# Performance work log

Measured on AMD Instinct MI355X. Metric: run time of the kernel, lower is better.

Reference implementation:

```python
import jax, jax.numpy as jnp
import numpy as np

EPS = 1e-12
B, C, H, M, E, P = 2, 20000, 64, 8, 200000, 3


def setup_inputs() -> dict:
    key = jax.random.key(0)
    ks = jax.random.split(key, 24)
    inp = {}
    inp["features"] = jax.random.normal(ks[0], (B, C, H), jnp.float32)
    inp["positions"] = jax.random.normal(ks[1], (B, C, P), jnp.float32)
    inp["edge_index"] = jax.random.randint(ks[2], (2, E), 0, C)
    inp["degree"] = jax.random.randint(ks[3], (C,), 1, 33).astype(jnp.float32)
    inp["cell_node_indices"] = jax.random.randint(ks[4], (C, M), 0, C)
    mask = (jax.random.uniform(ks[5], (C, M)) > 0.3).astype(jnp.float32)
    inp["cell_node_mask"] = mask.at[:, 0].set(1.0)  # first node always valid (pad semantics)

    def lin(k, fan_in, fan_out):
        return (jax.random.normal(k, (fan_in, fan_out), jnp.float32) / np.sqrt(fan_in)).astype(jnp.float32)

    # message MLP: Linear(2H+4 -> H), SiLU, Linear(H -> H)
    inp["W1"] = lin(ks[6], 2 * H + 4, H); inp["b1"] = jnp.zeros((H,), jnp.float32)
    inp["W2"] = lin(ks[7], H, H);         inp["b2"] = jnp.zeros((H,), jnp.float32)
    # position MLP: Linear(H -> H), SiLU, Linear(H -> 1)
    inp["P1"] = lin(ks[8], H, H);  inp["pb1"] = jnp.zeros((H,), jnp.float32)
    inp["P2"] = lin(ks[9], H, 1);  inp["pb2"] = jnp.zeros((1,), jnp.float32)
    # update MLP: Linear(2H -> H), SiLU, Linear(H -> H)
    inp["U1"] = lin(ks[10], 2 * H, H); inp["ub1"] = jnp.zeros((H,), jnp.float32)
    inp["U2"] = lin(ks[11], H, H);     inp["ub2"] = jnp.zeros((H,), jnp.float32)
    return inp


def _mlp(x, Wa, ba, Wb, bb):
    return jax.nn.silu(x @ Wa + ba) @ Wb + bb


def _forward(features, positions, edge_index, degree, cell_node_indices, cell_node_mask,
             W1, b1, W2, b2, P1, pb1, P2, pb2, U1, ub1, U2, ub2):
    src, dst = edge_index[0], edge_index[1]
    # gather padded node positions per cell: [B, C, M, P]
    node_pos = positions[:, cell_node_indices]

    h_src = features[:, src]                      # [B,E,H]
    h_dst = features[:, dst]
    rel = positions[:, src] - positions[:, dst]   # [B,E,P]
    dist = jnp.linalg.norm(rel, axis=-1, keepdims=True)  # [B,E,1]

    sp = node_pos[:, src]                         # [B,E,M,P]
    dp = node_pos[:, dst]
    mx = cell_node_mask[src]                      # [E,M]
    my = cell_node_mask[dst]

    # pairwise distances [B,E,M,M] via gram trick (avoids [B,E,M,M,P] intermediate)
    sp2 = jnp.sum(sp * sp, -1)                    # [B,E,M]
    dp2 = jnp.sum(dp * dp, -1)
    cross = jnp.einsum('bemp,benp->bemn', sp, dp)
    d = jnp.sqrt(jnp.maximum(sp2[..., :, None] + dp2[..., None, :] - 2.0 * cross, 0.0) + EPS)

    # masked pairwise-distance sum
    w = mx[:, :, None] * my[:, None, :]           # [E,M,M]
    pairwise = jnp.sum(d * w[None], axis=(-1, -2))  # [B,E]

    # centroid distance
    denx = jnp.maximum(mx.sum(-1, keepdims=True), EPS)  # [E,1]
    deny = jnp.maximum(my.sum(-1, keepdims=True), EPS)
    cx = jnp.sum(sp * mx[None, :, :, None], axis=2) / denx[None]  # [B,E,P]
    cy = jnp.sum(dp * my[None, :, :, None], axis=2) / deny[None]
    centroid = jnp.linalg.norm(cx - cy, axis=-1)  # [B,E]

    # Hausdorff distance (masked min/max)
    inf = jnp.float32(jnp.inf)
    d_xy = jnp.where(my[None, :, None, :] <= 0, inf, d)
    min_xy = jnp.where(mx[None] <= 0, 0.0, d_xy.min(-1))  # [B,E,M]
    h_xy = min_xy.max(-1)                                  # [B,E]
    d_yx = jnp.where(mx[None, :, None, :] <= 0, inf, jnp.swapaxes(d, -1, -2))
    min_yx = jnp.where(my[None] <= 0, 0.0, d_yx.min(-1))
    h_yx = min_yx.max(-1)
    haus = jnp.maximum(h_xy, h_yx)

    invariants = jnp.concatenate([dist, pairwise[..., None], centroid[..., None], haus[..., None]], -1)  # [B,E,4]
    msg_in = jnp.concatenate([h_src, h_dst, invariants], -1)  # [B,E,2H+4]
    messages = _mlp(msg_in, W1, b1, W2, b2)                   # [B,E,H]

    # scatter-aggregate into destination cells, degree-normalize
    agg = jnp.zeros_like(features).at[:, dst].add(messages)
    agg = agg / jnp.maximum(degree, 1.0)[None, :, None]

    # position update
    wts = jnp.tanh(_mlp(messages, P1, pb1, P2, pb2))          # [B,E,1]
    pos_upd = jnp.zeros_like(positions).at[:, dst].add(wts * rel)

    new_features = features + _mlp(jnp.concatenate([features, agg], -1), U1, ub1, U2, ub2)
    new_positions = positions + pos_upd
    return new_features, new_positions


def reference(features, positions, edge_index, degree, cell_node_indices, cell_node_mask,
              W1, b1, W2, b2, P1, pb1, P2, pb2, U1, ub1, U2, ub2):
    return _forward(features, positions, edge_index, degree, cell_node_indices, cell_node_mask,
                    W1, b1, W2, b2, P1, pb1, P2, pb2, U1, ub1, U2, ub2)
```

## Files before the change

kernel.cpp:

```cpp
#include <hip/hip_runtime.h>
#include <hip/hip_bf16.h>

#define B_ 2
#define C_ 20000
#define H_ 64
#define M_ 8
#define E_ 200000
#define P_ 3
#define EPS_ 1e-12f
#define ET_ (E_ / 64)

typedef __attribute__((ext_vector_type(8))) short short8;
typedef __attribute__((ext_vector_type(4))) float float4v;

__device__ __forceinline__ float silu_(float x) {
    return x / (1.f + __expf(-x));
}
__device__ __forceinline__ float tanh_fast_(float x) {
    float ex = __expf(2.f * x);
    return 1.f - 2.f / (ex + 1.f);
}
__device__ __forceinline__ unsigned short f2b(float f) {
    unsigned u = __float_as_uint(f);
    unsigned r = (u + 0x7FFF + ((u >> 16) & 1)) >> 16;
    return (unsigned short)r;
}
__device__ __forceinline__ float b2f(unsigned short h) {
    return __uint_as_float(((unsigned)h) << 16);
}
__device__ __forceinline__ unsigned pk2u(float a, float b) {
    __hip_bfloat162 h = __float22bfloat162_rn(make_float2(a, b));
    unsigned u; __builtin_memcpy(&u, &h, sizeof(u)); return u;
}
__device__ __forceinline__ float4 up4_(const unsigned short* p) {
    uint2 u = *(const uint2*)p;
    return make_float4(__uint_as_float(u.x << 16),
                       __uint_as_float(u.x & 0xffff0000u),
                       __uint_as_float(u.y << 16),
                       __uint_as_float(u.y & 0xffff0000u));
}

#define W1S_OFF 0
#define W2S_OFF 8192
#define P1S_OFF 12288
#define U1S_OFF 16384
#define U2S_OFF 24576
#define WBUF_ELEMS 28672

#define NB_PREP   120
#define NB_FEATB  2500
#define NB_DESC   157
#define NB_HIST   782
#define NB_COMBO  (NB_PREP + NB_FEATB + NB_DESC + NB_HIST)

#define NB_GEOM   6250
#define NB_AGGZ   2500
#define NB_PCPY   118
#define NB_GEOMK  (NB_GEOM + NB_AGGZ + NB_PCPY)

__global__ __launch_bounds__(256) void combo_kernel(
    const float* __restrict__ W1, const float* __restrict__ W2,
    const float* __restrict__ P1, const float* __restrict__ U1,
    const float* __restrict__ U2, unsigned short* __restrict__ wbuf,
    const float* __restrict__ feat, unsigned short* __restrict__ featb,
    const float* __restrict__ pos, const int* __restrict__ cni,
    const float* __restrict__ mask, unsigned short* __restrict__ descb,
    const int* __restrict__ ei, int* __restrict__ cnt)
{
    const int bid = blockIdx.x;
    if (bid < NB_PREP) {
        int t = bid * 256 + threadIdx.x;
        if (t >= WBUF_ELEMS) return;
        const float* W; int e;
        if (t < W2S_OFF)      { W = W1; e = t; }
        else if (t < U1S_OFF) { W = (t < P1S_OFF) ? W2 : P1; e = (t < P1S_OFF) ? t - W2S_OFF : t - P1S_OFF; }
        else if (t < U2S_OFF) { W = U1; e = t - U1S_OFF; }
        else                  { W = U2; e = t - U2S_OFF; }
        int j = e & 7, lane = (e >> 3) & 63, nt = (e >> 9) & 3, kk = e >> 11;
        int k = kk * 32 + ((lane >> 4) * 8) + j;
        int n = nt * 16 + (lane & 15);
        wbuf[t] = f2b(W[k * 64 + n]);
    } else if (bid < NB_PREP + NB_FEATB) {
        int t = (bid - NB_PREP) * 256 + threadIdx.x;
        float4 v = *(const float4*)&feat[(size_t)t * 4];
        *(uint2*)&featb[(size_t)t * 4] = make_uint2(pk2u(v.x, v.y), pk2u(v.z, v.w));
    } else if (bid < NB_PREP + NB_FEATB + NB_DESC) {
        int tid = (bid - NB_PREP - NB_FEATB) * 256 + threadIdx.x;
        if (tid >= B_ * C_) return;
        int b = tid / C_, c = tid - b * C_;
        const float* pb = pos + (size_t)b * C_ * P_;
        unsigned short* R = descb + (size_t)tid * 40;
        int4 n0 = *(const int4*)&cni[c*8];
        int4 n1 = *(const int4*)&cni[c*8 + 4];
        float4 m0 = *(const float4*)&mask[c*8];
        float4 m1 = *(const float4*)&mask[c*8 + 4];
        int ni[8] = {n0.x, n0.y, n0.z, n0.w, n1.x, n1.y, n1.z, n1.w};
        float mm[8] = {m0.x, m0.y, m0.z, m0.w, m1.x, m1.y, m1.z, m1.w};
        float sx = 0.f, sy = 0.f, sz = 0.f, sm = 0.f;
        #pragma unroll
        for (int m = 0; m < 8; ++m) {
            float x = pb[ni[m]*3+0], y = pb[ni[m]*3+1], z = pb[ni[m]*3+2];
            *(uint2*)&R[m*4] = make_uint2(pk2u(x, y), pk2u(z, mm[m]));
            sx += x * mm[m]; sy += y * mm[m]; sz += z * mm[m]; sm += mm[m];
        }
        float inv = 1.f / fmaxf(sm, EPS_);
        *(uint2*)&R[32] = make_uint2(pk2u(sx*inv, sy*inv), pk2u(sz*inv, sm));
        *(uint2*)&R[36] = make_uint2(pk2u(pb[c*3+0], pb[c*3+1]), pk2u(pb[c*3+2], 0.f));
    } else {
        int e = (bid - NB_PREP - NB_FEATB - NB_DESC) * 256 + threadIdx.x;
        if (e >= E_) return;
        atomicAdd(&cnt[ei[E_ + e]], 1);
    }
}

__global__ __launch_bounds__(256) void alloc_kernel(
    const int* __restrict__ cnt, int* __restrict__ cursor, int* __restrict__ total)
{
    int idx = blockIdx.x * 256 + threadIdx.x;
    int lane = threadIdx.x & 63;
    int v = (idx < C_) ? cnt[idx] : 0;
    int inc = v;
    #pragma unroll
    for (int s = 1; s < 64; s <<= 1) {
        int n = __shfl_up(inc, s);
        if (lane >= s) inc += n;
    }
    int wtot = __shfl(inc, 63);
    int base = 0;
    if (lane == 0) base = atomicAdd(total, wtot);
    base = __shfl(base, 0);
    if (idx < C_) cursor[idx] = base + inc - v;
}

__global__ __launch_bounds__(256) void scatter_kernel(
    const int* __restrict__ ei, int* __restrict__ cursor,
    int2* __restrict__ sedge)
{
    int e = blockIdx.x * 256 + threadIdx.x;
    if (e >= E_) return;
    int s = ei[e], d = ei[E_ + e];
    int slot = atomicAdd(&cursor[d], 1);
    sedge[slot] = make_int2(s, d);
}

__global__ __launch_bounds__(256) void geom_kernel(
    const int2* __restrict__ sedge, const unsigned short* __restrict__ descb,
    float* __restrict__ inv8,
    float* __restrict__ aggf, const float* __restrict__ pos,
    float* __restrict__ out_pos)
{
    const int bid = blockIdx.x;
    if (bid >= NB_GEOM) {
        if (bid < NB_GEOM + NB_AGGZ) {
            int t = (bid - NB_GEOM) * 256 + threadIdx.x;
            ((float4*)aggf)[t] = make_float4(0.f, 0.f, 0.f, 0.f);
        } else {
            int t = (bid - NB_GEOM - NB_AGGZ) * 256 + threadIdx.x;
            if (t < (B_ * C_ * P_) / 4)
                ((float4*)out_pos)[t] = ((const float4*)pos)[t];
        }
        return;
    }
    const int tid  = threadIdx.x;
    const int w    = tid >> 6;
    const int lane = tid & 63;
    const int q    = lane >> 4;
    const int l16  = lane & 15;

    const int ge = bid * 64 + w * 16 + l16;
    const int b  = ge / E_;
    const int i  = ge - b * E_;
    const int2 sd = sedge[i];
    const unsigned short* Sb = descb + ((size_t)b * C_ + sd.x) * 40;
    const unsigned short* Db = descb + ((size_t)b * C_ + sd.y) * 40;

    const float INFV = __builtin_inff();
    float4 S[8];
    float a_i[8], infm_i[8], rowmin[8];
    #pragma unroll
    for (int k = 0; k < 8; ++k) {
        S[k] = up4_(&Sb[k*4]);
        a_i[k] = S[k].x*S[k].x + S[k].y*S[k].y + S[k].z*S[k].z + EPS_;
        infm_i[k] = (S[k].w > 0.f) ? 0.f : INFV;
        rowmin[k] = INFV;
    }
    float pair = 0.f, hyx = 0.f;
    #pragma unroll
    for (int jj = 0; jj < 2; ++jj) {
        float4 Dj = up4_(&Db[(q*2 + jj)*4]);
        float dp2 = Dj.x*Dj.x + Dj.y*Dj.y + Dj.z*Dj.z;
        float infm_j = (Dj.w > 0.f) ? 0.f : INFV;
        float colmin = INFV, psum = 0.f;
        #pragma unroll
        for (int k = 0; k < 8; ++k) {
            float cr = S[k].x*Dj.x + S[k].y*Dj.y + S[k].z*Dj.z;
            float t  = (a_i[k] + dp2) - 2.f*cr;
            float dd = sqrtf(fmaxf(t, EPS_));
            psum = fmaf(dd, S[k].w, psum);
            rowmin[k] = fminf(rowmin[k], dd + infm_j);
            colmin    = fminf(colmin,    dd + infm_i[k]);
        }
        pair = fmaf(Dj.w, psum, pair);
        hyx = fmaxf(hyx, (Dj.w > 0.f) ? colmin : 0.f);
    }
    pair += __shfl_xor(pair, 16);  pair += __shfl_xor(pair, 32);
    hyx = fmaxf(hyx, __shfl_xor(hyx, 16));  hyx = fmaxf(hyx, __shfl_xor(hyx, 32));
    #pragma unroll
    for (int k = 0; k < 8; ++k) {
        rowmin[k] = fminf(rowmin[k], __shfl_xor(rowmin[k], 16));
        rowmin[k] = fminf(rowmin[k], __shfl_xor(rowmin[k], 32));
    }
    float hxy = 0.f;
    #pragma unroll
    for (int k = 0; k < 8; ++k)
        hxy = fmaxf(hxy, (S[k].w > 0.f) ? rowmin[k] : 0.f);

    float4 Sc = up4_(&Sb[32]), Dc = up4_(&Db[32]);
    float cdx = Sc.x - Dc.x, cdy = Sc.y - Dc.y, cdz = Sc.z - Dc.z;
    float4 Sp = up4_(&Sb[36]), Dp = up4_(&Db[36]);
    float relx = Sp.x - Dp.x, rely = Sp.y - Dp.y, relz = Sp.z - Dp.z;
    float dist = sqrtf(relx*relx + rely*rely + relz*relz);
    float cen  = sqrtf(cdx*cdx + cdy*cdy + cdz*cdz);
    float haus = fmaxf(hxy, hyx);

    size_t off = ((size_t)b * E_ + i) * 8;
    if (q == 0)      *(float4*)&inv8[off]     = make_float4(dist, pair, cen, haus);
    else if (q == 1) *(float4*)&inv8[off + 4] = make_float4(relx, rely, relz, 0.f);
}

__global__ __launch_bounds__(256) void edge_kernel(
    const unsigned short* __restrict__ featb,
    const int2* __restrict__ sedge, const float* __restrict__ inv8,
    const unsigned short* __restrict__ wbuf, const float* __restrict__ W1,
    const float* __restrict__ b1, const float* __restrict__ b2,
    const float* __restrict__ pb1, const float* __restrict__ P2,
    const float* __restrict__ pb2,
    float* __restrict__ aggf, float* __restrict__ out_pos)
{
    __shared__ unsigned short lds[4 * 3328];

    const int tid  = threadIdx.x;
    const int w    = tid >> 6;
    const int lane = tid & 63;
    const int q    = lane >> 4;
    const int l16  = lane & 15;
    const int w16  = w * 16;

    const int tile = blockIdx.x;
    const int b    = tile / ET_;
    const int i0   = (tile - b * ET_) * 64;
    const int2 sd  = sedge[i0 + lane];
    const int s_l  = sd.x;
    const int d_l  = sd.y;
    const unsigned short* fb = featb + (size_t)b * C_ * H_;
    const float* ivb = inv8 + ((size_t)b * E_ + i0) * 8;

    unsigned short* Xw = lds + w * 3328;
    unsigned short* Hw = Xw + 2176;
    unsigned short* Mw = Xw;

    float4 ivhi = *(const float4*)&ivb[(w16 + l16) * 8 + 4];
    const float relx = ivhi.x, rely = ivhi.y, relz = ivhi.z;

    const int rr4 = lane >> 4, c4 = lane & 15;
    #pragma unroll
    for (int it = 0; it < 4; ++it) {
        int rloc = it * 4 + rr4;
        int r = w16 + rloc;
        int sr = __shfl(s_l, r);
        int dr = __shfl(d_l, r);
        uint2 vs = *(const uint2*)&fb[(size_t)sr * 64 + c4 * 4];
        uint2 vd = *(const uint2*)&fb[(size_t)dr * 64 + c4 * 4];
        *(uint2*)&Xw[rloc*136 + c4*4]      = vs;
        *(uint2*)&Xw[rloc*136 + 64 + c4*4] = vd;
    }

    float4v acc[4];
    #pragma unroll
    for (int nt = 0; nt < 4; ++nt) {
        float bv = b1[nt*16 + l16];
        acc[nt] = (float4v){bv, bv, bv, bv};
    }
    #pragma unroll
    for (int kk = 0; kk < 4; ++kk) {
        short8 a = *(const short8*)&Xw[l16*136 + kk*32 + q*8];
        #pragma unroll
        for (int nt = 0; nt < 4; ++nt) {
            short8 bf = *(const short8*)&wbuf[W1S_OFF + (((kk*4 + nt)*64) + lane) * 8];
            acc[nt] = __builtin_amdgcn_mfma_f32_16x16x32_bf16(a, bf, acc[nt], 0, 0, 0);
        }
    }
    float4 iv[4];
    #pragma unroll
    for (int i = 0; i < 4; ++i)
        iv[i] = *(const float4*)&ivb[(w16 + q*4 + i) * 8];
    #pragma unroll
    for (int nt = 0; nt < 4; ++nt) {
        float wa = W1[128*64 + nt*16 + l16];
        float wb = W1[129*64 + nt*16 + l16];
        float wc = W1[130*64 + nt*16 + l16];
        float wd = W1[131*64 + nt*16 + l16];
        #pragma unroll
        for (int i = 0; i < 4; ++i)
            acc[nt][i] += iv[i].x*wa + iv[i].y*wb + iv[i].z*wc + iv[i].w*wd;
    }
    #pragma unroll
    for (int nt = 0; nt < 4; ++nt)
        #pragma unroll
        for (int i = 0; i < 4; ++i)
            Hw[(q*4 + i)*72 + nt*16 + l16] = f2b(silu_(acc[nt][i]));

    float4v mac[4];
    #pragma unroll
    for (int nt = 0; nt < 4; ++nt) {
        float bv = b2[nt*16 + l16];
        mac[nt] = (float4v){bv, bv, bv, bv};
    }
    #pragma unroll
    for (int kk = 0; kk < 2; ++kk) {
        short8 a = *(const short8*)&Hw[l16*72 + kk*32 + q*8];
        #pragma unroll
        for (int nt = 0; nt < 4; ++nt) {
            short8 bf = *(const short8*)&wbuf[W2S_OFF + (((kk*4 + nt)*64) + lane) * 8];
            mac[nt] = __builtin_amdgcn_mfma_f32_16x16x32_bf16(a, bf, mac[nt], 0, 0, 0);
        }
    }
    #pragma unroll
    for (int nt = 0; nt < 4; ++nt)
        #pragma unroll
        for (int i = 0; i < 4; ++i)
            Mw[(q*4 + i)*72 + nt*16 + l16] = f2b(mac[nt][i]);

    float4v gac[4];
    #pragma unroll
    for (int nt = 0; nt < 4; ++nt) {
        float bv = pb1[nt*16 + l16];
        gac[nt] = (float4v){bv, bv, bv, bv};
    }
    #pragma unroll
    for (int kk = 0; kk < 2; ++kk) {
        short8 a = *(const short8*)&Mw[l16*72 + kk*32 + q*8];
        #pragma unroll
        for (int nt = 0; nt < 4; ++nt) {
            short8 bf = *(const short8*)&wbuf[P1S_OFF + (((kk*4 + nt)*64) + lane) * 8];
            gac[nt] = __builtin_amdgcn_mfma_f32_16x16x32_bf16(a, bf, gac[nt], 0, 0, 0);
        }
    }
    float p2v[4];
    #pragma unroll
    for (int nt = 0; nt < 4; ++nt) p2v[nt] = P2[nt*16 + l16];
    const float pb2v = pb2[0];

    #pragma unroll
    for (int i = 0; i < 4; ++i) {
        float p = 0.f;
        #pragma unroll
        for (int nt = 0; nt < 4; ++nt) p += silu_(gac[nt][i]) * p2v[nt];
        p += __shfl_xor(p, 8);
        p += __shfl_xor(p, 4);
        p += __shfl_xor(p, 2);
        p += __shfl_xor(p, 1);
        float wt = tanh_fast_(p + pb2v);
        if (l16 == 0) *(float*)&Mw[(q*4 + i)*72 + 64] = wt;
    }

    float* aggB = aggf + (size_t)b * C_ * 64;
    float* opB  = out_pos + (size_t)b * C_ * 3;

    float mrow[16];
    #pragma unroll
    for (int rr = 0; rr < 16; ++rr) mrow[rr] = b2f(Mw[rr*72 + lane]);
    float wtl = *(const float*)&Mw[l16*72 + 64];

    int dprev = __shfl(d_l, w16);
    float colacc = 0.f, pxa = 0.f, pya = 0.f, pza = 0.f;
    #pragma unroll
    for (int rr = 0; rr < 16; ++rr) {
        int dcur = __shfl(d_l, w16 + rr);
        if (dcur != dprev) {
            atomicAdd(&aggB[(size_t)dprev * 64 + lane], colacc);
            if (lane < 3) {
                float v = (lane == 0) ? pxa : (lane == 1) ? pya : pza;
                atomicAdd(&opB[(size_t)dprev * 3 + lane], v);
            }
            colacc = 0.f; pxa = 0.f; pya = 0.f; pza = 0.f;
            dprev = dcur;
        }
        float wt = __shfl(wtl, rr);
        colacc += mrow[rr];
        pxa = fmaf(wt, __shfl(relx, rr), pxa);
        pya = fmaf(wt, __shfl(rely, rr), pya);
        pza = fmaf(wt, __shfl(relz, rr), pza);
    }
    atomicAdd(&aggB[(size_t)dprev * 64 + lane], colacc);
    if (lane < 3) {
        float v = (lane == 0) ? pxa : (lane == 1) ? pya : pza;
        atomicAdd(&opB[(size_t)dprev * 3 + lane], v);
    }
}

__global__ __launch_bounds__(256) void node_kernel(
    const float* __restrict__ feat, const unsigned short* __restrict__ featb,
    const float* __restrict__ aggf, const float* __restrict__ deg,
    const unsigned short* __restrict__ wbuf,
    const float* __restrict__ ub1, const float* __restrict__ ub2,
    float* __restrict__ out_feat)
{
    __shared__ unsigned short lds[4 * 3328];

    const int tid  = threadIdx.x;
    const int w    = tid >> 6;
    const int lane = tid & 63;
    const int q    = lane >> 4;
    const int l16  = lane & 15;
    const int g0   = blockIdx.x * 64;

    unsigned short* Xw = lds + w * 3328;
    unsigned short* Hw = Xw + 2176;

    const int rr4 = lane >> 4, c4 = lane & 15;
    #pragma unroll
    for (int it = 0; it < 4; ++it) {
        int rloc = it * 4 + rr4;
        int g = g0 + w*16 + rloc;
        int gc = (g >= C_) ? g - C_ : g;
        float sc = 1.f / fmaxf(deg[gc], 1.f);
        uint2  vf = *(const uint2*)&featb[(size_t)g * 64 + c4 * 4];
        float4 va = *(const float4*)&aggf[(size_t)g * 64 + c4 * 4];
        *(uint2*)&Xw[rloc*136 + c4*4]      = vf;
        *(uint2*)&Xw[rloc*136 + 64 + c4*4] =
            make_uint2(pk2u(va.x*sc, va.y*sc), pk2u(va.z*sc, va.w*sc));
    }

    float4v acc[4];
    #pragma unroll
    for (int nt = 0; nt < 4; ++nt) {
        float bv = ub1[nt*16 + l16];
        acc[nt] = (float4v){bv, bv, bv, bv};
    }
    #pragma unroll
    for (int kk = 0; kk < 4; ++kk) {
        short8 a = *(const short8*)&Xw[l16*136 + kk*32 + q*8];
        #pragma unroll
        for (int nt = 0; nt < 4; ++nt) {
            short8 bf = *(const short8*)&wbuf[U1S_OFF + (((kk*4 + nt)*64) + lane) * 8];
            acc[nt] = __builtin_amdgcn_mfma_f32_16x16x32_bf16(a, bf, acc[nt], 0, 0, 0);
        }
    }
    #pragma unroll
    for (int nt = 0; nt < 4; ++nt)
        #pragma unroll
        for (int i = 0; i < 4; ++i)
            Hw[(q*4 + i)*72 + nt*16 + l16] = f2b(silu_(acc[nt][i]));

    float4v oac[4];
    #pragma unroll
    for (int nt = 0; nt < 4; ++nt) {
        float bv = ub2[nt*16 + l16];
        oac[nt] = (float4v){bv, bv, bv, bv};
    }
    #pragma unroll
    for (int kk = 0; kk < 2; ++kk) {
        short8 a = *(const short8*)&Hw[l16*72 + kk*32 + q*8];
        #pragma unroll
        for (int nt = 0; nt < 4; ++nt) {
            short8 bf = *(const short8*)&wbuf[U2S_OFF + (((kk*4 + nt)*64) + lane) * 8];
            oac[nt] = __builtin_amdgcn_mfma_f32_16x16x32_bf16(a, bf, oac[nt], 0, 0, 0);
        }
    }
    #pragma unroll
    for (int nt = 0; nt < 4; ++nt)
        #pragma unroll
        for (int i = 0; i < 4; ++i) {
            size_t idx = (size_t)(g0 + w*16 + q*4 + i) * 64 + nt*16 + l16;
            out_feat[idx] = feat[idx] + oac[nt][i];
        }
}

extern "C" void kernel_launch(void* const* d_in, const int* in_sizes, int n_in,
                              void* d_out, int out_size, void* d_ws, size_t ws_size,
                              hipStream_t stream) {
    const float* feat = (const float*)d_in[0];
    const float* pos  = (const float*)d_in[1];
    const int*   ei   = (const int*)d_in[2];
    const float* deg  = (const float*)d_in[3];
    const int*   cni  = (const int*)d_in[4];
    const float* mask = (const float*)d_in[5];
    const float* W1   = (const float*)d_in[6];
    const float* b1   = (const float*)d_in[7];
    const float* W2   = (const float*)d_in[8];
    const float* b2   = (const float*)d_in[9];
    const float* P1   = (const float*)d_in[10];
    const float* pb1  = (const float*)d_in[11];
    const float* P2   = (const float*)d_in[12];
    const float* pb2  = (const float*)d_in[13];
    const float* U1   = (const float*)d_in[14];
    const float* ub1  = (const float*)d_in[15];
    const float* U2   = (const float*)d_in[16];
    const float* ub2  = (const float*)d_in[17];

    float* out_feat = (float*)d_out;
    float* out_pos  = out_feat + (size_t)B_ * C_ * H_;

    float* aggf = (float*)d_ws;
    unsigned short* featb = (unsigned short*)(aggf + (size_t)B_ * C_ * 64);
    unsigned short* descb = featb + (size_t)B_ * C_ * 64;
    unsigned short* wbuf  = descb + (size_t)B_ * C_ * 40;
    int* cnt    = (int*)(wbuf + WBUF_ELEMS);
    int* total  = cnt + C_;
    int* cursor = total + 4;
    int2* sedge = (int2*)(cursor + C_);
    float* inv8 = (float*)(sedge + E_);

    hipMemsetAsync(cnt, 0, (C_ + 4) * sizeof(int), stream);

    combo_kernel<<<NB_COMBO, 256, 0, stream>>>(
        W1, W2, P1, U1, U2, wbuf, feat, featb, pos, cni, mask, descb, ei, cnt);

    alloc_kernel<<<(C_ + 255) / 256, 256, 0, stream>>>(cnt, cursor, total);
    scatter_kernel<<<(E_ + 255) / 256, 256, 0, stream>>>(ei, cursor, sedge);

    geom_kernel<<<NB_GEOMK, 256, 0, stream>>>(sedge, descb, inv8, aggf, pos, out_pos);

    edge_kernel<<<B_ * ET_, 256, 0, stream>>>(
        featb, sedge, inv8, wbuf, W1, b1, b2, pb1, P2, pb2, aggf, out_pos);

    node_kernel<<<(B_ * C_) / 64, 256, 0, stream>>>(
        feat, featb, aggf, deg, wbuf, ub1, ub2, out_feat);
}
```

Measured before the change: 232.9 us.

## Fold W2·P1 into one weight, pad invariants into MFMA, segmented position scatter

The position MLP's first layer now uses a precomputed product W2·P1 (plus a folded bias b2·P1+pb1) applied directly to the hidden activations. This lets the gate MFMAs run in the same loop as the message MFMAs instead of waiting for the messages to be written back to LDS. The four invariant inputs are packed into a fifth zero-padded K-slice of the first MFMA, which replaces the scalar FMA tail that read W1 from global memory. The position scatter becomes a per-row segmented prefix sum with one atomic per segment instead of a serial shuffle loop. Messages are now kept in fp32 in LDS, which raises LDS use per block. Folding the weights in bf16 changes rounding.

```diff
diff --git a/kernel.cpp b/kernel.cpp
--- a/kernel.cpp
+++ b/kernel.cpp
@@ -41,17 +41,18 @@
 }
 
 #define W1S_OFF 0
-#define W2S_OFF 8192
-#define P1S_OFF 12288
-#define U1S_OFF 16384
-#define U2S_OFF 24576
-#define WBUF_ELEMS 28672
+#define W2S_OFF 10240
+#define P1S_OFF 14336
+#define U1S_OFF 18432
+#define U2S_OFF 26624
+#define WBUF_ELEMS 30720
 
 #define NB_PREP   120
 #define NB_FEATB  2500
 #define NB_DESC   157
 #define NB_HIST   782
-#define NB_COMBO  (NB_PREP + NB_FEATB + NB_DESC + NB_HIST)
+#define NB_GB     1
+#define NB_COMBO  (NB_PREP + NB_FEATB + NB_DESC + NB_HIST + NB_GB)
 
 #define NB_GEOM   6250
 #define NB_AGGZ   2500
@@ -65,21 +66,45 @@
     const float* __restrict__ feat, unsigned short* __restrict__ featb,
     const float* __restrict__ pos, const int* __restrict__ cni,
     const float* __restrict__ mask, unsigned short* __restrict__ descb,
-    const int* __restrict__ ei, int* __restrict__ cnt)
+    const int* __restrict__ ei, int* __restrict__ cnt,
+    const float* __restrict__ b2, const float* __restrict__ pb1,
+    float* __restrict__ gateb)
 {
     const int bid = blockIdx.x;
     if (bid < NB_PREP) {
         int t = bid * 256 + threadIdx.x;
         if (t >= WBUF_ELEMS) return;
-        const float* W; int e;
-        if (t < W2S_OFF)      { W = W1; e = t; }
-        else if (t < U1S_OFF) { W = (t < P1S_OFF) ? W2 : P1; e = (t < P1S_OFF) ? t - W2S_OFF : t - P1S_OFF; }
-        else if (t < U2S_OFF) { W = U1; e = t - U1S_OFF; }
-        else                  { W = U2; e = t - U2S_OFF; }
-        int j = e & 7, lane = (e >> 3) & 63, nt = (e >> 9) & 3, kk = e >> 11;
-        int k = kk * 32 + ((lane >> 4) * 8) + j;
-        int n = nt * 16 + (lane & 15);
-        wbuf[t] = f2b(W[k * 64 + n]);
+        int e;
+        int j, lane, nt, kk, k, n;
+        if (t < W2S_OFF) {
+            e = t;
+            j = e & 7; lane = (e >> 3) & 63; nt = (e >> 9) & 3; kk = e >> 11;
+            k = kk * 32 + ((lane >> 4) * 8) + j;
+            n = nt * 16 + (lane & 15);
+            wbuf[t] = f2b((k < 132) ? W1[k * 64 + n] : 0.f);
+        } else if (t < P1S_OFF) {
+            e = t - W2S_OFF;
+            j = e & 7; lane = (e >> 3) & 63; nt = (e >> 9) & 3; kk = e >> 11;
+            k = kk * 32 + ((lane >> 4) * 8) + j;
+            n = nt * 16 + (lane & 15);
+            wbuf[t] = f2b(W2[k * 64 + n]);
+        } else if (t < U1S_OFF) {
+            e = t - P1S_OFF;
+            j = e & 7; lane = (e >> 3) & 63; nt = (e >> 9) & 3; kk = e >> 11;
+            k = kk * 32 + ((lane >> 4) * 8) + j;
+            n = nt * 16 + (lane & 15);
+            float acc = 0.f;
+            for (int j2 = 0; j2 < 64; ++j2)
+                acc = fmaf(W2[k * 64 + j2], P1[j2 * 64 + n], acc);
+            wbuf[t] = f2b(acc);
+        } else {
+            const float* W = (t < U2S_OFF) ? U1 : U2;
+            e = (t < U2S_OFF) ? t - U1S_OFF : t - U2S_OFF;
+            j = e & 7; lane = (e >> 3) & 63; nt = (e >> 9) & 3; kk = e >> 11;
+            k = kk * 32 + ((lane >> 4) * 8) + j;
+            n = nt * 16 + (lane & 15);
+            wbuf[t] = f2b(W[k * 64 + n]);
+        }
     } else if (bid < NB_PREP + NB_FEATB) {
         int t = (bid - NB_PREP) * 256 + threadIdx.x;
         float4 v = *(const float4*)&feat[(size_t)t * 4];
@@ -106,10 +131,17 @@
         float inv = 1.f / fmaxf(sm, EPS_);
         *(uint2*)&R[32] = make_uint2(pk2u(sx*inv, sy*inv), pk2u(sz*inv, sm));
         *(uint2*)&R[36] = make_uint2(pk2u(pb[c*3+0], pb[c*3+1]), pk2u(pb[c*3+2], 0.f));
-    } else {
+    } else if (bid < NB_PREP + NB_FEATB + NB_DESC + NB_HIST) {
         int e = (bid - NB_PREP - NB_FEATB - NB_DESC) * 256 + threadIdx.x;
         if (e >= E_) return;
         atomicAdd(&cnt[ei[E_ + e]], 1);
+    } else {
+        int n = threadIdx.x;
+        if (n >= 64) return;
+        float acc = pb1[n];
+        for (int j = 0; j < 64; ++j)
+            acc = fmaf(b2[j], P1[j * 64 + n], acc);
+        gateb[n] = acc;
     }
 }
 
@@ -231,13 +263,13 @@
 __global__ __launch_bounds__(256) void edge_kernel(
     const unsigned short* __restrict__ featb,
     const int2* __restrict__ sedge, const float* __restrict__ inv8,
-    const unsigned short* __restrict__ wbuf, const float* __restrict__ W1,
+    const unsigned short* __restrict__ wbuf,
     const float* __restrict__ b1, const float* __restrict__ b2,
-    const float* __restrict__ pb1, const float* __restrict__ P2,
+    const float* __restrict__ gateb, const float* __restrict__ P2,
     const float* __restrict__ pb2,
     float* __restrict__ aggf, float* __restrict__ out_pos)
 {
-    __shared__ unsigned short lds[4 * 3328];
+    __shared__ unsigned short lds[4 * 3840];
 
     const int tid  = threadIdx.x;
     const int w    = tid >> 6;
@@ -255,9 +287,9 @@
     const unsigned short* fb = featb + (size_t)b * C_ * H_;
     const float* ivb = inv8 + ((size_t)b * E_ + i0) * 8;
 
-    unsigned short* Xw = lds + w * 3328;
-    unsigned short* Hw = Xw + 2176;
-    unsigned short* Mw = Xw;
+    unsigned short* Xw = lds + w * 3840;
+    unsigned short* Hw = Xw + 2688;
+    float* Mw = (float*)Xw;
 
     float4 ivhi = *(const float4*)&ivb[(w16 + l16) * 8 + 4];
     const float relx = ivhi.x, rely = ivhi.y, relz = ivhi.z;
@@ -271,8 +303,16 @@
         int dr = __shfl(d_l, r);
         uint2 vs = *(const uint2*)&fb[(size_t)sr * 64 + c4 * 4];
         uint2 vd = *(const uint2*)&fb[(size_t)dr * 64 + c4 * 4];
-        *(uint2*)&Xw[rloc*136 + c4*4]      = vs;
-        *(uint2*)&Xw[rloc*136 + 64 + c4*4] = vd;
+        *(uint2*)&Xw[rloc*168 + c4*4]      = vs;
+        *(uint2*)&Xw[rloc*168 + 64 + c4*4] = vd;
+        if (c4 < 8) {
+            uint2 vz = make_uint2(0u, 0u);
+            if (c4 == 0) {
+                float4 iv = *(const float4*)&ivb[r * 8];
+                vz = make_uint2(pk2u(iv.x, iv.y), pk2u(iv.z, iv.w));
+            }
+            *(uint2*)&Xw[rloc*168 + 128 + c4*4] = vz;
+        }
     }
 
     float4v acc[4];
@@ -282,39 +322,27 @@
         acc[nt] = (float4v){bv, bv, bv, bv};
     }
     #pragma unroll
-    for (int kk = 0; kk < 4; ++kk) {
-        short8 a = *(const short8*)&Xw[l16*136 + kk*32 + q*8];
+    for (int kk = 0; kk < 5; ++kk) {
+        short8 a = *(const short8*)&Xw[l16*168 + kk*32 + q*8];
         #pragma unroll
         for (int nt = 0; nt < 4; ++nt) {
             short8 bf = *(const short8*)&wbuf[W1S_OFF + (((kk*4 + nt)*64) + lane) * 8];
             acc[nt] = __builtin_amdgcn_mfma_f32_16x16x32_bf16(a, bf, acc[nt], 0, 0, 0);
         }
     }
-    float4 iv[4];
-    #pragma unroll
-    for (int i = 0; i < 4; ++i)
-        iv[i] = *(const float4*)&ivb[(w16 + q*4 + i) * 8];
-    #pragma unroll
-    for (int nt = 0; nt < 4; ++nt) {
-        float wa = W1[128*64 + nt*16 + l16];
-        float wb = W1[129*64 + nt*16 + l16];
-        float wc = W1[130*64 + nt*16 + l16];
-        float wd = W1[131*64 + nt*16 + l16];
-        #pragma unroll
-        for (int i = 0; i < 4; ++i)
-            acc[nt][i] += iv[i].x*wa + iv[i].y*wb + iv[i].z*wc + iv[i].w*wd;
-    }
     #pragma unroll
     for (int nt = 0; nt < 4; ++nt)
         #pragma unroll
         for (int i = 0; i < 4; ++i)
             Hw[(q*4 + i)*72 + nt*16 + l16] = f2b(silu_(acc[nt][i]));
 
-    float4v mac[4];
+    float4v mac[4], gac[4];
     #pragma unroll
     for (int nt = 0; nt < 4; ++nt) {
         float bv = b2[nt*16 + l16];
+        float gv = gateb[nt*16 + l16];
         mac[nt] = (float4v){bv, bv, bv, bv};
+        gac[nt] = (float4v){gv, gv, gv, gv};
     }
     #pragma unroll
     for (int kk = 0; kk < 2; ++kk) {
@@ -324,33 +352,25 @@
             short8 bf = *(const short8*)&wbuf[W2S_OFF + (((kk*4 + nt)*64) + lane) * 8];
             mac[nt] = __builtin_amdgcn_mfma_f32_16x16x32_bf16(a, bf, mac[nt], 0, 0, 0);
         }
-    }
-    #pragma unroll
-    for (int nt = 0; nt < 4; ++nt)
-        #pragma unroll
-        for (int i = 0; i < 4; ++i)
-            Mw[(q*4 + i)*72 + nt*16 + l16] = f2b(mac[nt][i]);
-
-    float4v gac[4];
-    #pragma unroll
-    for (int nt = 0; nt < 4; ++nt) {
-        float bv = pb1[nt*16 + l16];
-        gac[nt] = (float4v){bv, bv, bv, bv};
-    }
-    #pragma unroll
-    for (int kk = 0; kk < 2; ++kk) {
-        short8 a = *(const short8*)&Mw[l16*72 + kk*32 + q*8];
         #pragma unroll
         for (int nt = 0; nt < 4; ++nt) {
             short8 bf = *(const short8*)&wbuf[P1S_OFF + (((kk*4 + nt)*64) + lane) * 8];
             gac[nt] = __builtin_amdgcn_mfma_f32_16x16x32_bf16(a, bf, gac[nt], 0, 0, 0);
         }
     }
+
+    #pragma unroll
+    for (int nt = 0; nt < 4; ++nt)
+        #pragma unroll
+        for (int i = 0; i < 4; ++i)
+            Mw[(q*4 + i)*68 + nt*16 + l16] = mac[nt][i];
+
     float p2v[4];
     #pragma unroll
     for (int nt = 0; nt < 4; ++nt) p2v[nt] = P2[nt*16 + l16];
     const float pb2v = pb2[0];
 
+    float wt_i[4];
     #pragma unroll
     for (int i = 0; i < 4; ++i) {
         float p = 0.f;
@@ -360,43 +380,55 @@
         p += __shfl_xor(p, 4);
         p += __shfl_xor(p, 2);
         p += __shfl_xor(p, 1);
-        float wt = tanh_fast_(p + pb2v);
-        if (l16 == 0) *(float*)&Mw[(q*4 + i)*72 + 64] = wt;
-    }
+        wt_i[i] = tanh_fast_(p + pb2v);
+    }
+    int in_ = l16 & 3, qn = l16 >> 2;
+    float wtsel = wt_i[0];
+    wtsel = (in_ == 1) ? wt_i[1] : wtsel;
+    wtsel = (in_ == 2) ? wt_i[2] : wtsel;
+    wtsel = (in_ == 3) ? wt_i[3] : wtsel;
+    const float wtl = __shfl(wtsel, (qn << 4) | in_);
 
     float* aggB = aggf + (size_t)b * C_ * 64;
     float* opB  = out_pos + (size_t)b * C_ * 3;
 
+    int dl  = __shfl(d_l, w16 + l16);
+    int dnx = __shfl(d_l, w16 + ((l16 + 1) & 15));
+    bool isEnd = (l16 == 15) || (dl != dnx);
+    unsigned long long bm = __ballot(isEnd);
+    unsigned grp16 = (unsigned)bm & 0xFFFFu;
+
+    float gv = wtl * ((q == 0) ? relx : (q == 1) ? rely : relz);
+    float Pf = gv;
+    #pragma unroll
+    for (int s = 1; s < 16; s <<= 1) {
+        float n = __shfl_up(Pf, s);
+        Pf += (l16 >= s) ? n : 0.f;
+    }
+    unsigned below = grp16 & ((1u << l16) - 1u);
+    int pe = 31 - __clz(below | 1u);
+    float Pp = __shfl(Pf, (lane & 48) + pe);
+    float segsum = Pf - ((below != 0u) ? Pp : 0.f);
+    if (isEnd && q < 3)
+        atomicAdd(&opB[(size_t)dl * 3 + q], segsum);
+
     float mrow[16];
     #pragma unroll
-    for (int rr = 0; rr < 16; ++rr) mrow[rr] = b2f(Mw[rr*72 + lane]);
-    float wtl = *(const float*)&Mw[l16*72 + 64];
+    for (int rr = 0; rr < 16; ++rr) mrow[rr] = Mw[rr*68 + lane];
 
     int dprev = __shfl(d_l, w16);
-    float colacc = 0.f, pxa = 0.f, pya = 0.f, pza = 0.f;
+    float colacc = 0.f;
     #pragma unroll
     for (int rr = 0; rr < 16; ++rr) {
         int dcur = __shfl(d_l, w16 + rr);
         if (dcur != dprev) {
             atomicAdd(&aggB[(size_t)dprev * 64 + lane], colacc);
-            if (lane < 3) {
-                float v = (lane == 0) ? pxa : (lane == 1) ? pya : pza;
-                atomicAdd(&opB[(size_t)dprev * 3 + lane], v);
-            }
-            colacc = 0.f; pxa = 0.f; pya = 0.f; pza = 0.f;
+            colacc = 0.f;
             dprev = dcur;
         }
-        float wt = __shfl(wtl, rr);
         colacc += mrow[rr];
-        pxa = fmaf(wt, __shfl(relx, rr), pxa);
-        pya = fmaf(wt, __shfl(rely, rr), pya);
-        pza = fmaf(wt, __shfl(relz, rr), pza);
     }
     atomicAdd(&aggB[(size_t)dprev * 64 + lane], colacc);
-    if (lane < 3) {
-        float v = (lane == 0) ? pxa : (lane == 1) ? pya : pza;
-        atomicAdd(&opB[(size_t)dprev * 3 + lane], v);
-    }
 }
 
 __global__ __launch_bounds__(256) void node_kernel(
@@ -506,7 +538,8 @@
     unsigned short* featb = (unsigned short*)(aggf + (size_t)B_ * C_ * 64);
     unsigned short* descb = featb + (size_t)B_ * C_ * 64;
     unsigned short* wbuf  = descb + (size_t)B_ * C_ * 40;
-    int* cnt    = (int*)(wbuf + WBUF_ELEMS);
+    float* gateb = (float*)(wbuf + WBUF_ELEMS);
+    int* cnt    = (int*)(gateb + 64);
     int* total  = cnt + C_;
     int* cursor = total + 4;
     int2* sedge = (int2*)(cursor + C_);
@@ -515,7 +548,8 @@
     hipMemsetAsync(cnt, 0, (C_ + 4) * sizeof(int), stream);
 
     combo_kernel<<<NB_COMBO, 256, 0, stream>>>(
-        W1, W2, P1, U1, U2, wbuf, feat, featb, pos, cni, mask, descb, ei, cnt);
+        W1, W2, P1, U1, U2, wbuf, feat, featb, pos, cni, mask, descb, ei, cnt,
+        b2, pb1, gateb);
 
     alloc_kernel<<<(C_ + 255) / 256, 256, 0, stream>>>(cnt, cursor, total);
     scatter_kernel<<<(E_ + 255) / 256, 256, 0, stream>>>(ei, cursor, sedge);
@@ -523,7 +557,7 @@
     geom_kernel<<<NB_GEOMK, 256, 0, stream>>>(sedge, descb, inv8, aggf, pos, out_pos);
 
     edge_kernel<<<B_ * ET_, 256, 0, stream>>>(
-        featb, sedge, inv8, wbuf, W1, b1, b2, pb1, P2, pb2, aggf, out_pos);
+        featb, sedge, inv8, wbuf, b1, b2, gateb, P2, pb2, aggf, out_pos);
 
     node_kernel<<<(B_ * C_) / 64, 256, 0, stream>>>(
         feat, featb, aggf, deg, wbuf, ub1, ub2, out_feat);
```

Result: no change. 229.0 us (-1.7%).
